# Performance work log

Measured on AMD Instinct MI355X. Metric: run time of the kernel, lower is better.

## Reference

```python
import jax, jax.numpy as jnp
import numpy as np

N_FFT = 1024
FREQ = N_FFT // 2 + 1          # 513
FRAMES = 256
WIN_MIN = 10.0                 # max(1, n_fft//100)
WIN_MAX = 1024.0               # n_fft
HOP_MIN = 1.0
HOP_MAX = 256.0
EPS = 1e-12
SIG_LEN = int(HOP_MAX) * FRAMES + N_FFT  # 66560


def setup_inputs() -> dict:
    key = jax.random.key(0)
    k1, k2, k3 = jax.random.split(key, 3)
    x = jax.random.normal(k1, (4, SIG_LEN), dtype=jnp.float32)
    raw_win_length = jax.random.normal(k2, (FREQ,), dtype=jnp.float32)
    raw_hop_length = jax.random.normal(k3, (1,), dtype=jnp.float32)
    return {"x": x, "raw_win_length": raw_win_length, "raw_hop_length": raw_hop_length}


def reference(x, raw_win_length, raw_hop_length):
    B, L = x.shape
    dt = x.dtype
    # sigmoid reparameterization (matches logit init in __init__)
    hop = HOP_MIN + jax.nn.sigmoid(raw_hop_length[0]) * (HOP_MAX - HOP_MIN)      # scalar
    theta = WIN_MIN + jax.nn.sigmoid(raw_win_length) * (WIN_MAX - WIN_MIN)

    # fractional frame positions: integer floor for gather, differentiable frac
    t = jnp.arange(FRAMES, dtype=dt)
    pos = jnp.clip(t * hop, 0.0, float(L - N_FFT))                               # [T]
    idx_floor = jnp.floor(pos).astype(jnp.int32)                                 # [T] (non-diff)
    idx_frac = pos - idx_floor.astype(dt)                                        # [T] (diff: d/dhop = t)

    # unfold: frames[b,t,n] = x[b, idx_floor[t] + n]
    n = jnp.arange(N_FFT)
    frames = x[:, idx_floor[:, None] + n[None, :]]                               # [B,T,N]

    # fractionally-shifted, per-frequency-length hann window: [F,T,N]
    nf = n.astype(dt)
    d = nf[None, :] - (N_FFT - 1) / 2.0 - idx_frac[:, None]                      # [T,N] offset from true center
    th = theta[:, None, None]                                                    # [F,1,1]
    w = jnp.where(jnp.abs(d)[None] <= th / 2.0,
                  0.5 + 0.5 * jnp.cos(2.0 * jnp.pi * d[None] / th),
                  0.0)                                                           # [F,T,N]

    # direct DFT (window varies per freq bin -> no FFT possible)
    k = jnp.arange(FREQ, dtype=dt)
    ang = 2.0 * jnp.pi * k[:, None] * nf[None, :] / N_FFT                        # [F,N]
    re = jnp.einsum('btn,ftn,fn->bft', frames, w, jnp.cos(ang))
    im = -jnp.einsum('btn,ftn,fn->bft', frames, w, jnp.sin(ang))
    stft = jax.lax.complex(re, im)                                               # [B,F,T]
    spec = jnp.abs(stft) + EPS                                                   # magnitude_power = 1
    return spec, stft
```

## Files before the change

### kernel.cpp

```cpp
#include <hip/hip_runtime.h>
#include <math.h>

#define NFFT   1024
#define FREQ   513
#define FRAMES 256
#define SIGLEN 66560
#define NB     4
#define BFT    (NB * FREQ * FRAMES)
#define NWAVE  4
#define NTHR   (64 * NWAVE)
#define NCHUNK 9
#define UNITS  (NCHUNK * FRAMES)

typedef float f32x2 __attribute__((ext_vector_type(2)));

__device__ __forceinline__ float sigmoid_f32(float v)
{
    if (v >= 0.0f) {
        return 1.0f / (1.0f + expf(-v));
    } else {
        const float e = expf(v);
        return e / (1.0f + e);
    }
}

__device__ __forceinline__ float rfl_f32(float v)
{
    return __int_as_float(__builtin_amdgcn_readfirstlane(__float_as_int(v)));
}

__global__ __launch_bounds__(1024)
void dstft_setup(const float* __restrict__ raw_win,
                 const float* __restrict__ raw_hop,
                 unsigned short* __restrict__ sf,
                 float* __restrict__ ctmax,
                 int* __restrict__ tbase,
                 float* __restrict__ tc)
{
    __shared__ float th[FREQ];
    const int tid = threadIdx.x;
    if (tid < FREQ)
        th[tid] = 10.0f + sigmoid_f32(raw_win[tid]) * 1014.0f;
    __syncthreads();
    if (tid < FREQ) {
        const float ti = th[tid];
        int r = 0;
        for (int j = 0; j < FREQ; ++j) {
            const float tj = th[j];
            r += (tj > ti) || (tj == ti && j < tid);
        }
        sf[r] = (unsigned short)tid;
        if ((r & 63) == 0) ctmax[r >> 6] = ti;
    }
    if (tid < FRAMES) {
        const float hop = 1.0f + sigmoid_f32(raw_hop[0]) * 255.0f;
        float pos = (float)tid * hop;
        pos = fminf(fmaxf(pos, 0.0f), 65536.0f);
        const float fl = floorf(pos);
        tbase[tid] = (int)fl;
        tc[tid]    = 511.5f + (pos - fl);
    }
}

__global__ __launch_bounds__(NTHR, 8)
void dstft_main(const float* __restrict__ x,
                const float* __restrict__ raw_win,
                const float* __restrict__ raw_hop,
                const unsigned short* __restrict__ sf,
                const float* __restrict__ ctmax,
                const int* __restrict__ tbase,
                const float* __restrict__ tc,
                float* __restrict__ out, int out_size, int stft_mode)
{
    const int tid  = threadIdx.x;
    const int lane = tid & 63;
    const int q    = tid >> 6;

    __shared__ __align__(16) unsigned char smem[NFFT * sizeof(float4)];
    float4* xlds = reinterpret_cast<float4*>(smem);
    float (*part)[64][9] = reinterpret_cast<float (*)[64][9]>(smem);

    const int u     = (int)blockIdx.x;
    const int chunk = u >> 8;
    const int t     = u & 255;
    const int spos  = chunk * 64 + lane;
    const bool active = (spos < FREQ);

    int   f = 0;
    float theta, tmax, c;
    int   base;

    if (sf) {
        if (active) {
            f = (int)sf[spos];
            f = (f < 0) ? 0 : ((f > FREQ - 1) ? (FREQ - 1) : f);
        }
        theta = active ? (10.0f + sigmoid_f32(raw_win[f]) * 1014.0f) : 10.0f;
        tmax  = rfl_f32(ctmax[chunk]);
        base  = __builtin_amdgcn_readfirstlane(tbase[t]);
        c     = rfl_f32(tc[t]);
    } else {
        if (active) f = spos;
        theta = active ? (10.0f + sigmoid_f32(raw_win[f]) * 1014.0f) : 10.0f;
        float tmaxv = theta;
#pragma unroll
        for (int s = 32; s; s >>= 1)
            tmaxv = fmaxf(tmaxv, __shfl_xor(tmaxv, s, 64));
        tmax = rfl_f32(tmaxv);
        const float hop = 1.0f + sigmoid_f32(raw_hop[0]) * 255.0f;
        float pos = (float)t * hop;
        pos = fminf(fmaxf(pos, 0.0f), 65536.0f);
        const float fl = floorf(pos);
        base = __builtin_amdgcn_readfirstlane((int)fl);
        c    = rfl_f32(511.5f + (pos - fl));
    }

    int lo = (int)floorf(c - 0.5f * tmax);
    int hi = (int)ceilf (c + 0.5f * tmax);
    lo = lo > 0 ? lo : 0;
    hi = hi < (NFFT - 1) ? hi : (NFFT - 1);
    int cnt = hi - lo + 1;
    cnt = cnt < 0 ? 0 : (cnt > NFFT ? NFFT : cnt);
    lo  = __builtin_amdgcn_readfirstlane(lo);
    cnt = __builtin_amdgcn_readfirstlane(cnt);

    for (int n = lo + tid; n < lo + cnt; n += NTHR) {
        float4 v;
        v.x = x[base + n];
        v.y = x[base + n + SIGLEN];
        v.z = x[base + n + 2 * SIGLEN];
        v.w = x[base + n + 3 * SIGLEN];
        xlds[n - lo] = v;
    }
    __syncthreads();

    const int s0     = lo + (cnt * q) / NWAVE;
    const int s1     = lo + (cnt * (q + 1)) / NWAVE;
    const int segcnt = s1 - s0;

    const float invth = 1.0f / theta;
    float r = ((float)s0 - c) * invth;

    const float sdr = (float)f * (1.0f / 1024.0f);
    const float cd  = __builtin_amdgcn_cosf(sdr);
    const float sd  = __builtin_amdgcn_sinf(sdr);
    int m0 = (f * s0) & (NFFT - 1);
    m0 = (m0 >= 512) ? (m0 - 1024) : m0;
    const float p0 = (float)m0 * (1.0f / 1024.0f);

    f32x2 p;
    p.x = __builtin_amdgcn_cosf(p0);
    p.y = __builtin_amdgcn_sinf(p0);
    const f32x2 cdv = { cd,  cd };
    const f32x2 sdv = { -sd, sd };

    f32x2 are01 = {0.f, 0.f}, are23 = {0.f, 0.f};
    f32x2 aim01 = {0.f, 0.f}, aim23 = {0.f, 0.f};

    const float4* __restrict__ xp = &xlds[s0 - lo];
#pragma unroll 4
    for (int i = 0; i < segcnt; ++i) {
        const float rc = __builtin_amdgcn_fmed3f(r, -0.5f, 0.5f);
        const float w  = fmaf(0.5f, __builtin_amdgcn_cosf(rc), 0.5f);
        const float wc  = w * p.x;
        const float wsn = w * p.y;
        const f32x2 wcv = { wc,  wc  };
        const f32x2 wsv = { wsn, wsn };
        const float4 v = xp[i];
        const f32x2 v01 = { v.x, v.y };
        const f32x2 v23 = { v.z, v.w };
        are01 = __builtin_elementwise_fma(v01, wcv, are01);
        are23 = __builtin_elementwise_fma(v23, wcv, are23);
        aim01 = __builtin_elementwise_fma(v01, wsv, aim01);
        aim23 = __builtin_elementwise_fma(v23, wsv, aim23);
        const f32x2 ps = p.yx;
        p = __builtin_elementwise_fma(p, cdv, ps * sdv);
        r += invth;
    }

    __syncthreads();
    part[q][lane][0] = are01.x;  part[q][lane][1] = are01.y;
    part[q][lane][2] = are23.x;  part[q][lane][3] = are23.y;
    part[q][lane][4] = aim01.x;  part[q][lane][5] = aim01.y;
    part[q][lane][6] = aim23.x;  part[q][lane][7] = aim23.y;
    __syncthreads();

    if (active) {
        float res = 0.f, sms = 0.f;
#pragma unroll
        for (int pw = 0; pw < NWAVE; ++pw) {
            res += part[pw][lane][q];
            sms += part[pw][lane][4 + q];
        }
        const float re = res;
        const float im = -sms;
        const int idx = q * (FREQ * FRAMES) + f * FRAMES + t;
        if (idx < out_size)
            out[idx] = sqrtf(fmaf(re, re, im * im)) + 1e-12f;
        if (stft_mode == 2) {
            if (BFT + 2 * idx + 1 < out_size) {
                out[BFT + 2 * idx]     = re;
                out[BFT + 2 * idx + 1] = im;
            }
        } else {
            if (BFT + idx < out_size)
                out[BFT + idx] = re;
        }
    }
}

extern "C" void kernel_launch(void* const* d_in, const int* in_sizes, int n_in,
                              void* d_out, int out_size, void* d_ws, size_t ws_size,
                              hipStream_t stream)
{
    const float* x       = (const float*)d_in[0];
    const float* raw_win = (const float*)d_in[1];
    const float* raw_hop = (const float*)d_in[2];
    float* out = (float*)d_out;

    unsigned short* sf    = nullptr;
    float*          ctmax = nullptr;
    int*            tbase = nullptr;
    float*          tc    = nullptr;
    if (d_ws != nullptr && ws_size >= 3200) {
        sf    = (unsigned short*)d_ws;
        ctmax = (float*)((char*)d_ws + 1028);
        tbase = (int*)  ((char*)d_ws + 1064);
        tc    = (float*)((char*)d_ws + 2088);
        dstft_setup<<<1, 1024, 0, stream>>>(raw_win, raw_hop,
                                            sf, ctmax, tbase, tc);
    }
    const int stft_mode = (out_size >= 3 * BFT) ? 2 : 1;
    dstft_main<<<UNITS, NTHR, 0, stream>>>(
        x, raw_win, raw_hop, sf, ctmax, tbase, tc, out, out_size, stft_mode);
}
```

Baseline: 56.83 us.

## Process two adjacent frames per block over a shared union span

Each block now computes two consecutive frames. It loads the union of both frames' sample ranges into LDS once, and a single twiddle recurrence indexed by absolute sample position is shared by both frames. Each frame's phase is then corrected by a per-frame rotation in the epilogue. This halves the grid and reuses the LDS loads and twiddle work across frames. In exchange, both frames iterate over the whole union span, which includes samples that fall outside one frame's window, so per-element cosine work doubles. The span is also clamped to 1280 entries, which could truncate data if the hop is near its maximum.

```diff
diff --git a/kernel.cpp b/kernel.cpp
--- a/kernel.cpp
+++ b/kernel.cpp
@@ -10,7 +10,9 @@
 #define NWAVE  4
 #define NTHR   (64 * NWAVE)
 #define NCHUNK 9
-#define UNITS  (NCHUNK * FRAMES)
+#define NPAIR  (FRAMES / 2)
+#define GRIDP  (NCHUNK * NPAIR)
+#define MAXU   1280
 
 typedef float f32x2 __attribute__((ext_vector_type(2)));
 
@@ -76,19 +78,20 @@
     const int lane = tid & 63;
     const int q    = tid >> 6;
 
-    __shared__ __align__(16) unsigned char smem[NFFT * sizeof(float4)];
+    __shared__ __align__(16) unsigned char smem[MAXU * sizeof(float4)];
     float4* xlds = reinterpret_cast<float4*>(smem);
-    float (*part)[64][9] = reinterpret_cast<float (*)[64][9]>(smem);
+    float (*part)[64][17] = reinterpret_cast<float (*)[64][17]>(smem);
 
     const int u     = (int)blockIdx.x;
-    const int chunk = u >> 8;
-    const int t     = u & 255;
+    const int chunk = u >> 7;
+    const int tp    = u & (NPAIR - 1);
+    const int t0    = 2 * tp, t1 = t0 + 1;
     const int spos  = chunk * 64 + lane;
     const bool active = (spos < FREQ);
 
     int   f = 0;
-    float theta, tmax, c;
-    int   base;
+    float theta, tmax, c0, c1;
+    int   base0, base1;
 
     if (sf) {
         if (active) {
@@ -97,8 +100,10 @@
         }
         theta = active ? (10.0f + sigmoid_f32(raw_win[f]) * 1014.0f) : 10.0f;
         tmax  = rfl_f32(ctmax[chunk]);
-        base  = __builtin_amdgcn_readfirstlane(tbase[t]);
-        c     = rfl_f32(tc[t]);
+        base0 = __builtin_amdgcn_readfirstlane(tbase[t0]);
+        base1 = __builtin_amdgcn_readfirstlane(tbase[t1]);
+        c0    = rfl_f32(tc[t0]);
+        c1    = rfl_f32(tc[t1]);
     } else {
         if (active) f = spos;
         theta = active ? (10.0f + sigmoid_f32(raw_win[f]) * 1014.0f) : 10.0f;
@@ -108,43 +113,49 @@
             tmaxv = fmaxf(tmaxv, __shfl_xor(tmaxv, s, 64));
         tmax = rfl_f32(tmaxv);
         const float hop = 1.0f + sigmoid_f32(raw_hop[0]) * 255.0f;
-        float pos = (float)t * hop;
-        pos = fminf(fmaxf(pos, 0.0f), 65536.0f);
-        const float fl = floorf(pos);
-        base = __builtin_amdgcn_readfirstlane((int)fl);
-        c    = rfl_f32(511.5f + (pos - fl));
-    }
-
-    int lo = (int)floorf(c - 0.5f * tmax);
-    int hi = (int)ceilf (c + 0.5f * tmax);
-    lo = lo > 0 ? lo : 0;
-    hi = hi < (NFFT - 1) ? hi : (NFFT - 1);
-    int cnt = hi - lo + 1;
-    cnt = cnt < 0 ? 0 : (cnt > NFFT ? NFFT : cnt);
-    lo  = __builtin_amdgcn_readfirstlane(lo);
-    cnt = __builtin_amdgcn_readfirstlane(cnt);
-
-    for (int n = lo + tid; n < lo + cnt; n += NTHR) {
+        float pos0 = fminf(fmaxf((float)t0 * hop, 0.0f), 65536.0f);
+        float pos1 = fminf(fmaxf((float)t1 * hop, 0.0f), 65536.0f);
+        const float fl0 = floorf(pos0), fl1 = floorf(pos1);
+        base0 = __builtin_amdgcn_readfirstlane((int)fl0);
+        base1 = __builtin_amdgcn_readfirstlane((int)fl1);
+        c0    = rfl_f32(511.5f + (pos0 - fl0));
+        c1    = rfl_f32(511.5f + (pos1 - fl1));
+    }
+
+    int lo0 = (int)floorf(c0 - 0.5f * tmax);
+    int hi1 = (int)ceilf (c1 + 0.5f * tmax);
+    lo0 = lo0 > 0 ? lo0 : 0;
+    hi1 = hi1 < (NFFT - 1) ? hi1 : (NFFT - 1);
+    int gmin = base0 + lo0;
+    int gmax = base1 + hi1;
+    int cntU = gmax - gmin + 1;
+    cntU = cntU < 1 ? 1 : (cntU > MAXU ? MAXU : cntU);
+    gmin = __builtin_amdgcn_readfirstlane(gmin);
+    cntU = __builtin_amdgcn_readfirstlane(cntU);
+
+    for (int n = tid; n < cntU; n += NTHR) {
         float4 v;
-        v.x = x[base + n];
-        v.y = x[base + n + SIGLEN];
-        v.z = x[base + n + 2 * SIGLEN];
-        v.w = x[base + n + 3 * SIGLEN];
-        xlds[n - lo] = v;
-    }
-    __syncthreads();
-
-    const int s0     = lo + (cnt * q) / NWAVE;
-    const int s1     = lo + (cnt * (q + 1)) / NWAVE;
-    const int segcnt = s1 - s0;
+        v.x = x[gmin + n];
+        v.y = x[gmin + n + SIGLEN];
+        v.z = x[gmin + n + 2 * SIGLEN];
+        v.w = x[gmin + n + 3 * SIGLEN];
+        xlds[n] = v;
+    }
+    __syncthreads();
+
+    const int si     = (cntU * q) / NWAVE;
+    const int si1    = (cntU * (q + 1)) / NWAVE;
+    const int segcnt = si1 - si;
+    const int sg     = gmin + si;
 
     const float invth = 1.0f / theta;
-    float r = ((float)s0 - c) * invth;
+    float r0 = ((float)(sg - base0) - c0) * invth;
+    float r1 = ((float)(sg - base1) - c1) * invth;
 
     const float sdr = (float)f * (1.0f / 1024.0f);
     const float cd  = __builtin_amdgcn_cosf(sdr);
     const float sd  = __builtin_amdgcn_sinf(sdr);
-    int m0 = (f * s0) & (NFFT - 1);
+    int m0 = (f * sg) & (NFFT - 1);
     m0 = (m0 >= 512) ? (m0 - 1024) : m0;
     const float p0 = (float)m0 * (1.0f / 1024.0f);
 
@@ -154,57 +165,78 @@
     const f32x2 cdv = { cd,  cd };
     const f32x2 sdv = { -sd, sd };
 
-    f32x2 are01 = {0.f, 0.f}, are23 = {0.f, 0.f};
-    f32x2 aim01 = {0.f, 0.f}, aim23 = {0.f, 0.f};
-
-    const float4* __restrict__ xp = &xlds[s0 - lo];
-#pragma unroll 4
+    f32x2 cr0a = {0,0}, cr0b = {0,0}, sr0a = {0,0}, sr0b = {0,0};
+    f32x2 cr1a = {0,0}, cr1b = {0,0}, sr1a = {0,0}, sr1b = {0,0};
+
+    const float4* __restrict__ xp = &xlds[si];
+#pragma unroll 2
     for (int i = 0; i < segcnt; ++i) {
-        const float rc = __builtin_amdgcn_fmed3f(r, -0.5f, 0.5f);
-        const float w  = fmaf(0.5f, __builtin_amdgcn_cosf(rc), 0.5f);
-        const float wc  = w * p.x;
-        const float wsn = w * p.y;
-        const f32x2 wcv = { wc,  wc  };
-        const f32x2 wsv = { wsn, wsn };
+        const float rc0 = __builtin_amdgcn_fmed3f(r0, -0.5f, 0.5f);
+        const float w0  = fmaf(0.5f, __builtin_amdgcn_cosf(rc0), 0.5f);
+        const float rc1 = __builtin_amdgcn_fmed3f(r1, -0.5f, 0.5f);
+        const float w1  = fmaf(0.5f, __builtin_amdgcn_cosf(rc1), 0.5f);
         const float4 v = xp[i];
-        const f32x2 v01 = { v.x, v.y };
-        const f32x2 v23 = { v.z, v.w };
-        are01 = __builtin_elementwise_fma(v01, wcv, are01);
-        are23 = __builtin_elementwise_fma(v23, wcv, are23);
-        aim01 = __builtin_elementwise_fma(v01, wsv, aim01);
-        aim23 = __builtin_elementwise_fma(v23, wsv, aim23);
+        const f32x2 va = { v.x, v.y };
+        const f32x2 vb = { v.z, v.w };
+        const float wc0 = w0 * p.x, ws0 = w0 * p.y;
+        const float wc1 = w1 * p.x, ws1 = w1 * p.y;
+        const f32x2 wc0v = { wc0, wc0 }, ws0v = { ws0, ws0 };
+        const f32x2 wc1v = { wc1, wc1 }, ws1v = { ws1, ws1 };
+        cr0a = __builtin_elementwise_fma(va, wc0v, cr0a);
+        cr0b = __builtin_elementwise_fma(vb, wc0v, cr0b);
+        sr0a = __builtin_elementwise_fma(va, ws0v, sr0a);
+        sr0b = __builtin_elementwise_fma(vb, ws0v, sr0b);
+        cr1a = __builtin_elementwise_fma(va, wc1v, cr1a);
+        cr1b = __builtin_elementwise_fma(vb, wc1v, cr1b);
+        sr1a = __builtin_elementwise_fma(va, ws1v, sr1a);
+        sr1b = __builtin_elementwise_fma(vb, ws1v, sr1b);
         const f32x2 ps = p.yx;
         p = __builtin_elementwise_fma(p, cdv, ps * sdv);
-        r += invth;
-    }
-
-    __syncthreads();
-    part[q][lane][0] = are01.x;  part[q][lane][1] = are01.y;
-    part[q][lane][2] = are23.x;  part[q][lane][3] = are23.y;
-    part[q][lane][4] = aim01.x;  part[q][lane][5] = aim01.y;
-    part[q][lane][6] = aim23.x;  part[q][lane][7] = aim23.y;
+        r0 += invth;
+        r1 += invth;
+    }
+
+    __syncthreads();
+    part[q][lane][0]  = cr0a.x;  part[q][lane][1]  = cr0a.y;
+    part[q][lane][2]  = cr0b.x;  part[q][lane][3]  = cr0b.y;
+    part[q][lane][4]  = sr0a.x;  part[q][lane][5]  = sr0a.y;
+    part[q][lane][6]  = sr0b.x;  part[q][lane][7]  = sr0b.y;
+    part[q][lane][8]  = cr1a.x;  part[q][lane][9]  = cr1a.y;
+    part[q][lane][10] = cr1b.x;  part[q][lane][11] = cr1b.y;
+    part[q][lane][12] = sr1a.x;  part[q][lane][13] = sr1a.y;
+    part[q][lane][14] = sr1b.x;  part[q][lane][15] = sr1b.y;
     __syncthreads();
 
     if (active) {
-        float res = 0.f, sms = 0.f;
 #pragma unroll
-        for (int pw = 0; pw < NWAVE; ++pw) {
-            res += part[pw][lane][q];
-            sms += part[pw][lane][4 + q];
-        }
-        const float re = res;
-        const float im = -sms;
-        const int idx = q * (FREQ * FRAMES) + f * FRAMES + t;
-        if (idx < out_size)
-            out[idx] = sqrtf(fmaf(re, re, im * im)) + 1e-12f;
-        if (stft_mode == 2) {
-            if (BFT + 2 * idx + 1 < out_size) {
-                out[BFT + 2 * idx]     = re;
-                out[BFT + 2 * idx + 1] = im;
+        for (int k = 0; k < 2; ++k) {
+            float cr = 0.f, sr = 0.f;
+#pragma unroll
+            for (int pw = 0; pw < NWAVE; ++pw) {
+                cr += part[pw][lane][8 * k + q];
+                sr += part[pw][lane][8 * k + 4 + q];
             }
-        } else {
-            if (BFT + idx < out_size)
-                out[BFT + idx] = re;
+            const int bk = k ? base1 : base0;
+            int mk = (f * bk) & (NFFT - 1);
+            mk = (mk >= 512) ? (mk - 1024) : mk;
+            const float ph = (float)mk * (1.0f / 1024.0f);
+            const float cph = __builtin_amdgcn_cosf(ph);
+            const float sph = __builtin_amdgcn_sinf(ph);
+            const float re = cr * cph + sr * sph;
+            const float im = cr * sph - sr * cph;
+            const int tk  = k ? t1 : t0;
+            const int idx = q * (FREQ * FRAMES) + f * FRAMES + tk;
+            if (idx < out_size)
+                out[idx] = sqrtf(fmaf(re, re, im * im)) + 1e-12f;
+            if (stft_mode == 2) {
+                if (BFT + 2 * idx + 1 < out_size) {
+                    out[BFT + 2 * idx]     = re;
+                    out[BFT + 2 * idx + 1] = im;
+                }
+            } else {
+                if (BFT + idx < out_size)
+                    out[BFT + idx] = re;
+            }
         }
     }
 }
@@ -231,6 +263,6 @@
                                             sf, ctmax, tbase, tc);
     }
     const int stft_mode = (out_size >= 3 * BFT) ? 2 : 1;
-    dstft_main<<<UNITS, NTHR, 0, stream>>>(
+    dstft_main<<<GRIDP, NTHR, 0, stream>>>(
         x, raw_win, raw_hop, sf, ctmax, tbase, tc, out, out_size, stft_mode);
 }
```

New measurement: 67.71 us. 19.2% more time.

## Replace LDS staging of signal with per-wave global loads and readlane broadcast

Applied to the files above, without the earlier changes.

Removes the LDS staging buffer and the block barrier that followed the cooperative load. Each wave now loads 64 consecutive samples for all four batches into registers and broadcasts them to every lane with readlane inside a fully unrolled 64-step loop. Groups of 64 samples are interleaved across waves, and the twiddle phase is re-seeded with cos/sin at the start of each group. In exchange it adds four readlane ops per sample, drops the packed 2-wide FMAs, and the last partial group runs full 64-step iterations on clamped duplicate samples.

```diff
diff --git a/kernel.cpp b/kernel.cpp
--- a/kernel.cpp
+++ b/kernel.cpp
@@ -12,8 +12,6 @@
 #define NCHUNK 9
 #define UNITS  (NCHUNK * FRAMES)
 
-typedef float f32x2 __attribute__((ext_vector_type(2)));
-
 __device__ __forceinline__ float sigmoid_f32(float v)
 {
     if (v >= 0.0f) {
@@ -27,6 +25,11 @@
 __device__ __forceinline__ float rfl_f32(float v)
 {
     return __int_as_float(__builtin_amdgcn_readfirstlane(__float_as_int(v)));
+}
+
+__device__ __forceinline__ float rdlane_f32(float v, int k)
+{
+    return __uint_as_float(__builtin_amdgcn_readlane(__float_as_uint(v), k));
 }
 
 __global__ __launch_bounds__(1024)
@@ -76,9 +79,7 @@
     const int lane = tid & 63;
     const int q    = tid >> 6;
 
-    __shared__ __align__(16) unsigned char smem[NFFT * sizeof(float4)];
-    float4* xlds = reinterpret_cast<float4*>(smem);
-    float (*part)[64][9] = reinterpret_cast<float (*)[64][9]>(smem);
+    __shared__ float part[NWAVE][64][9];
 
     const int u     = (int)blockIdx.x;
     const int chunk = u >> 8;
@@ -123,66 +124,60 @@
     cnt = cnt < 0 ? 0 : (cnt > NFFT ? NFFT : cnt);
     lo  = __builtin_amdgcn_readfirstlane(lo);
     cnt = __builtin_amdgcn_readfirstlane(cnt);
-
-    for (int n = lo + tid; n < lo + cnt; n += NTHR) {
-        float4 v;
-        v.x = x[base + n];
-        v.y = x[base + n + SIGLEN];
-        v.z = x[base + n + 2 * SIGLEN];
-        v.w = x[base + n + 3 * SIGLEN];
-        xlds[n - lo] = v;
-    }
-    __syncthreads();
-
-    const int s0     = lo + (cnt * q) / NWAVE;
-    const int s1     = lo + (cnt * (q + 1)) / NWAVE;
-    const int segcnt = s1 - s0;
+    const int his = lo + cnt - 1;
+    const int G   = (cnt + 63) >> 6;
 
     const float invth = 1.0f / theta;
-    float r = ((float)s0 - c) * invth;
-
     const float sdr = (float)f * (1.0f / 1024.0f);
     const float cd  = __builtin_amdgcn_cosf(sdr);
     const float sd  = __builtin_amdgcn_sinf(sdr);
-    int m0 = (f * s0) & (NFFT - 1);
-    m0 = (m0 >= 512) ? (m0 - 1024) : m0;
-    const float p0 = (float)m0 * (1.0f / 1024.0f);
-
-    f32x2 p;
-    p.x = __builtin_amdgcn_cosf(p0);
-    p.y = __builtin_amdgcn_sinf(p0);
-    const f32x2 cdv = { cd,  cd };
-    const f32x2 sdv = { -sd, sd };
-
-    f32x2 are01 = {0.f, 0.f}, are23 = {0.f, 0.f};
-    f32x2 aim01 = {0.f, 0.f}, aim23 = {0.f, 0.f};
-
-    const float4* __restrict__ xp = &xlds[s0 - lo];
-#pragma unroll 4
-    for (int i = 0; i < segcnt; ++i) {
-        const float rc = __builtin_amdgcn_fmed3f(r, -0.5f, 0.5f);
-        const float w  = fmaf(0.5f, __builtin_amdgcn_cosf(rc), 0.5f);
-        const float wc  = w * p.x;
-        const float wsn = w * p.y;
-        const f32x2 wcv = { wc,  wc  };
-        const f32x2 wsv = { wsn, wsn };
-        const float4 v = xp[i];
-        const f32x2 v01 = { v.x, v.y };
-        const f32x2 v23 = { v.z, v.w };
-        are01 = __builtin_elementwise_fma(v01, wcv, are01);
-        are23 = __builtin_elementwise_fma(v23, wcv, are23);
-        aim01 = __builtin_elementwise_fma(v01, wsv, aim01);
-        aim23 = __builtin_elementwise_fma(v23, wsv, aim23);
-        const f32x2 ps = p.yx;
-        p = __builtin_elementwise_fma(p, cdv, ps * sdv);
-        r += invth;
-    }
-
-    __syncthreads();
-    part[q][lane][0] = are01.x;  part[q][lane][1] = are01.y;
-    part[q][lane][2] = are23.x;  part[q][lane][3] = are23.y;
-    part[q][lane][4] = aim01.x;  part[q][lane][5] = aim01.y;
-    part[q][lane][6] = aim23.x;  part[q][lane][7] = aim23.y;
+
+    float re0 = 0.f, re1 = 0.f, re2 = 0.f, re3 = 0.f;
+    float im0 = 0.f, im1 = 0.f, im2 = 0.f, im3 = 0.f;
+
+#pragma unroll 1
+    for (int g = q; g < G; g += NWAVE) {
+        const int sg = lo + (g << 6);
+        int sidx = sg + lane;
+        sidx = sidx < his ? sidx : his;
+        const float* __restrict__ xa = x + base + sidx;
+        const float xb0 = xa[0];
+        const float xb1 = xa[SIGLEN];
+        const float xb2 = xa[2 * SIGLEN];
+        const float xb3 = xa[3 * SIGLEN];
+
+        const float rg = ((float)sg - c) * invth;
+        int m0 = (f * sg) & (NFFT - 1);
+        m0 = (m0 >= 512) ? (m0 - 1024) : m0;
+        const float p0 = (float)m0 * (1.0f / 1024.0f);
+        float pc = __builtin_amdgcn_cosf(p0);
+        float ps = __builtin_amdgcn_sinf(p0);
+
+#pragma unroll
+        for (int k = 0; k < 64; ++k) {
+            const float x0 = rdlane_f32(xb0, k);
+            const float x1 = rdlane_f32(xb1, k);
+            const float x2 = rdlane_f32(xb2, k);
+            const float x3 = rdlane_f32(xb3, k);
+            const float rk = fmaf((float)k, invth, rg);
+            const float rc = __builtin_amdgcn_fmed3f(rk, -0.5f, 0.5f);
+            const float w  = fmaf(0.5f, __builtin_amdgcn_cosf(rc), 0.5f);
+            const float wc = w * pc;
+            const float ws = w * ps;
+            re0 = fmaf(x0, wc, re0);  im0 = fmaf(x0, ws, im0);
+            re1 = fmaf(x1, wc, re1);  im1 = fmaf(x1, ws, im1);
+            re2 = fmaf(x2, wc, re2);  im2 = fmaf(x2, ws, im2);
+            re3 = fmaf(x3, wc, re3);  im3 = fmaf(x3, ws, im3);
+            const float npc = fmaf(pc, cd, -(ps * sd));
+            const float nps = fmaf(ps, cd,   pc * sd);
+            pc = npc; ps = nps;
+        }
+    }
+
+    part[q][lane][0] = re0;  part[q][lane][1] = re1;
+    part[q][lane][2] = re2;  part[q][lane][3] = re3;
+    part[q][lane][4] = im0;  part[q][lane][5] = im1;
+    part[q][lane][6] = im2;  part[q][lane][7] = im3;
     __syncthreads();
 
     if (active) {
```

Result: slower. 71.73 us (+26.2%).

## Use persistent blocks with an atomic work counter for dynamic load balancing

Applied to the files above, without the earlier changes.

Launches a fixed grid of 2048 persistent blocks that pull (chunk, frame) work units from a global atomic counter, which the setup kernel initialises. Units with wide windows cost far more than narrow ones, so dynamic scheduling is meant to even out the tail and cut block launch overhead. It adds an atomic per unit and an extra barrier per iteration, and relies on the workspace being present.

```diff
diff --git a/kernel.cpp b/kernel.cpp
--- a/kernel.cpp
+++ b/kernel.cpp
@@ -11,6 +11,7 @@
 #define NTHR   (64 * NWAVE)
 #define NCHUNK 9
 #define UNITS  (NCHUNK * FRAMES)
+#define GRIDD  2048
 
 typedef float f32x2 __attribute__((ext_vector_type(2)));
 
@@ -35,10 +36,12 @@
                  unsigned short* __restrict__ sf,
                  float* __restrict__ ctmax,
                  int* __restrict__ tbase,
-                 float* __restrict__ tc)
+                 float* __restrict__ tc,
+                 int* __restrict__ counter)
 {
     __shared__ float th[FREQ];
     const int tid = threadIdx.x;
+    if (tid == 0) *counter = GRIDD;
     if (tid < FREQ)
         th[tid] = 10.0f + sigmoid_f32(raw_win[tid]) * 1014.0f;
     __syncthreads();
@@ -70,6 +73,7 @@
                 const float* __restrict__ ctmax,
                 const int* __restrict__ tbase,
                 const float* __restrict__ tc,
+                int* __restrict__ counter,
                 float* __restrict__ out, int out_size, int stft_mode)
 {
     const int tid  = threadIdx.x;
@@ -79,133 +83,149 @@
     __shared__ __align__(16) unsigned char smem[NFFT * sizeof(float4)];
     float4* xlds = reinterpret_cast<float4*>(smem);
     float (*part)[64][9] = reinterpret_cast<float (*)[64][9]>(smem);
-
-    const int u     = (int)blockIdx.x;
-    const int chunk = u >> 8;
-    const int t     = u & 255;
-    const int spos  = chunk * 64 + lane;
-    const bool active = (spos < FREQ);
-
-    int   f = 0;
-    float theta, tmax, c;
-    int   base;
-
-    if (sf) {
+    __shared__ int u_next[2];
+
+    const bool dyn = (counter != nullptr);
+    int u   = (int)blockIdx.x;
+    int tog = 0;
+
+    while (u < UNITS) {
+        if (dyn && tid == 0) u_next[tog] = atomicAdd(counter, 1);
+
+        const int chunk = u >> 8;
+        const int t     = u & 255;
+        const int spos  = chunk * 64 + lane;
+        const bool active = (spos < FREQ);
+
+        int   f = 0;
+        float theta, tmax, c;
+        int   base;
+
+        if (sf) {
+            if (active) {
+                f = (int)sf[spos];
+                f = (f < 0) ? 0 : ((f > FREQ - 1) ? (FREQ - 1) : f);
+            }
+            theta = active ? (10.0f + sigmoid_f32(raw_win[f]) * 1014.0f)
+                           : 10.0f;
+            tmax  = rfl_f32(ctmax[chunk]);
+            base  = __builtin_amdgcn_readfirstlane(tbase[t]);
+            c     = rfl_f32(tc[t]);
+        } else {
+            if (active) f = spos;
+            theta = active ? (10.0f + sigmoid_f32(raw_win[f]) * 1014.0f)
+                           : 10.0f;
+            float tmaxv = theta;
+#pragma unroll
+            for (int s = 32; s; s >>= 1)
+                tmaxv = fmaxf(tmaxv, __shfl_xor(tmaxv, s, 64));
+            tmax = rfl_f32(tmaxv);
+            const float hop = 1.0f + sigmoid_f32(raw_hop[0]) * 255.0f;
+            float pos = (float)t * hop;
+            pos = fminf(fmaxf(pos, 0.0f), 65536.0f);
+            const float fl = floorf(pos);
+            base = __builtin_amdgcn_readfirstlane((int)fl);
+            c    = rfl_f32(511.5f + (pos - fl));
+        }
+
+        int lo = (int)floorf(c - 0.5f * tmax);
+        int hi = (int)ceilf (c + 0.5f * tmax);
+        lo = lo > 0 ? lo : 0;
+        hi = hi < (NFFT - 1) ? hi : (NFFT - 1);
+        int cnt = hi - lo + 1;
+        cnt = cnt < 0 ? 0 : (cnt > NFFT ? NFFT : cnt);
+        lo  = __builtin_amdgcn_readfirstlane(lo);
+        cnt = __builtin_amdgcn_readfirstlane(cnt);
+
+        __syncthreads();
+
+        for (int n = lo + tid; n < lo + cnt; n += NTHR) {
+            float4 v;
+            v.x = x[base + n];
+            v.y = x[base + n + SIGLEN];
+            v.z = x[base + n + 2 * SIGLEN];
+            v.w = x[base + n + 3 * SIGLEN];
+            xlds[n - lo] = v;
+        }
+        __syncthreads();
+
+        const int s0     = lo + (cnt * q) / NWAVE;
+        const int s1     = lo + (cnt * (q + 1)) / NWAVE;
+        const int segcnt = s1 - s0;
+
+        const float invth = 1.0f / theta;
+        float r = ((float)s0 - c) * invth;
+
+        const float sdr = (float)f * (1.0f / 1024.0f);
+        const float cd  = __builtin_amdgcn_cosf(sdr);
+        const float sd  = __builtin_amdgcn_sinf(sdr);
+        int m0 = (f * s0) & (NFFT - 1);
+        m0 = (m0 >= 512) ? (m0 - 1024) : m0;
+        const float p0 = (float)m0 * (1.0f / 1024.0f);
+
+        f32x2 p;
+        p.x = __builtin_amdgcn_cosf(p0);
+        p.y = __builtin_amdgcn_sinf(p0);
+        const f32x2 cdv = { cd,  cd };
+        const f32x2 sdv = { -sd, sd };
+
+        f32x2 are01 = {0.f, 0.f}, are23 = {0.f, 0.f};
+        f32x2 aim01 = {0.f, 0.f}, aim23 = {0.f, 0.f};
+
+        const float4* __restrict__ xp = &xlds[s0 - lo];
+#pragma unroll 4
+        for (int i = 0; i < segcnt; ++i) {
+            const float rc = __builtin_amdgcn_fmed3f(r, -0.5f, 0.5f);
+            const float w  = fmaf(0.5f, __builtin_amdgcn_cosf(rc), 0.5f);
+            const float wc  = w * p.x;
+            const float wsn = w * p.y;
+            const f32x2 wcv = { wc,  wc  };
+            const f32x2 wsv = { wsn, wsn };
+            const float4 v = xp[i];
+            const f32x2 v01 = { v.x, v.y };
+            const f32x2 v23 = { v.z, v.w };
+            are01 = __builtin_elementwise_fma(v01, wcv, are01);
+            are23 = __builtin_elementwise_fma(v23, wcv, are23);
+            aim01 = __builtin_elementwise_fma(v01, wsv, aim01);
+            aim23 = __builtin_elementwise_fma(v23, wsv, aim23);
+            const f32x2 ps = p.yx;
+            p = __builtin_elementwise_fma(p, cdv, ps * sdv);
+            r += invth;
+        }
+
+        __syncthreads();
+        part[q][lane][0] = are01.x;  part[q][lane][1] = are01.y;
+        part[q][lane][2] = are23.x;  part[q][lane][3] = are23.y;
+        part[q][lane][4] = aim01.x;  part[q][lane][5] = aim01.y;
+        part[q][lane][6] = aim23.x;  part[q][lane][7] = aim23.y;
+        __syncthreads();
+
         if (active) {
-            f = (int)sf[spos];
-            f = (f < 0) ? 0 : ((f > FREQ - 1) ? (FREQ - 1) : f);
-        }
-        theta = active ? (10.0f + sigmoid_f32(raw_win[f]) * 1014.0f) : 10.0f;
-        tmax  = rfl_f32(ctmax[chunk]);
-        base  = __builtin_amdgcn_readfirstlane(tbase[t]);
-        c     = rfl_f32(tc[t]);
-    } else {
-        if (active) f = spos;
-        theta = active ? (10.0f + sigmoid_f32(raw_win[f]) * 1014.0f) : 10.0f;
-        float tmaxv = theta;
+            float res = 0.f, sms = 0.f;
 #pragma unroll
-        for (int s = 32; s; s >>= 1)
-            tmaxv = fmaxf(tmaxv, __shfl_xor(tmaxv, s, 64));
-        tmax = rfl_f32(tmaxv);
-        const float hop = 1.0f + sigmoid_f32(raw_hop[0]) * 255.0f;
-        float pos = (float)t * hop;
-        pos = fminf(fmaxf(pos, 0.0f), 65536.0f);
-        const float fl = floorf(pos);
-        base = __builtin_amdgcn_readfirstlane((int)fl);
-        c    = rfl_f32(511.5f + (pos - fl));
-    }
-
-    int lo = (int)floorf(c - 0.5f * tmax);
-    int hi = (int)ceilf (c + 0.5f * tmax);
-    lo = lo > 0 ? lo : 0;
-    hi = hi < (NFFT - 1) ? hi : (NFFT - 1);
-    int cnt = hi - lo + 1;
-    cnt = cnt < 0 ? 0 : (cnt > NFFT ? NFFT : cnt);
-    lo  = __builtin_amdgcn_readfirstlane(lo);
-    cnt = __builtin_amdgcn_readfirstlane(cnt);
-
-    for (int n = lo + tid; n < lo + cnt; n += NTHR) {
-        float4 v;
-        v.x = x[base + n];
-        v.y = x[base + n + SIGLEN];
-        v.z = x[base + n + 2 * SIGLEN];
-        v.w = x[base + n + 3 * SIGLEN];
-        xlds[n - lo] = v;
-    }
-    __syncthreads();
-
-    const int s0     = lo + (cnt * q) / NWAVE;
-    const int s1     = lo + (cnt * (q + 1)) / NWAVE;
-    const int segcnt = s1 - s0;
-
-    const float invth = 1.0f / theta;
-    float r = ((float)s0 - c) * invth;
-
-    const float sdr = (float)f * (1.0f / 1024.0f);
-    const float cd  = __builtin_amdgcn_cosf(sdr);
-    const float sd  = __builtin_amdgcn_sinf(sdr);
-    int m0 = (f * s0) & (NFFT - 1);
-    m0 = (m0 >= 512) ? (m0 - 1024) : m0;
-    const float p0 = (float)m0 * (1.0f / 1024.0f);
-
-    f32x2 p;
-    p.x = __builtin_amdgcn_cosf(p0);
-    p.y = __builtin_amdgcn_sinf(p0);
-    const f32x2 cdv = { cd,  cd };
-    const f32x2 sdv = { -sd, sd };
-
-    f32x2 are01 = {0.f, 0.f}, are23 = {0.f, 0.f};
-    f32x2 aim01 = {0.f, 0.f}, aim23 = {0.f, 0.f};
-
-    const float4* __restrict__ xp = &xlds[s0 - lo];
-#pragma unroll 4
-    for (int i = 0; i < segcnt; ++i) {
-        const float rc = __builtin_amdgcn_fmed3f(r, -0.5f, 0.5f);
-        const float w  = fmaf(0.5f, __builtin_amdgcn_cosf(rc), 0.5f);
-        const float wc  = w * p.x;
-        const float wsn = w * p.y;
-        const f32x2 wcv = { wc,  wc  };
-        const f32x2 wsv = { wsn, wsn };
-        const float4 v = xp[i];
-        const f32x2 v01 = { v.x, v.y };
-        const f32x2 v23 = { v.z, v.w };
-        are01 = __builtin_elementwise_fma(v01, wcv, are01);
-        are23 = __builtin_elementwise_fma(v23, wcv, are23);
-        aim01 = __builtin_elementwise_fma(v01, wsv, aim01);
-        aim23 = __builtin_elementwise_fma(v23, wsv, aim23);
-        const f32x2 ps = p.yx;
-        p = __builtin_elementwise_fma(p, cdv, ps * sdv);
-        r += invth;
-    }
-
-    __syncthreads();
-    part[q][lane][0] = are01.x;  part[q][lane][1] = are01.y;
-    part[q][lane][2] = are23.x;  part[q][lane][3] = are23.y;
-    part[q][lane][4] = aim01.x;  part[q][lane][5] = aim01.y;
-    part[q][lane][6] = aim23.x;  part[q][lane][7] = aim23.y;
-    __syncthreads();
-
-    if (active) {
-        float res = 0.f, sms = 0.f;
-#pragma unroll
-        for (int pw = 0; pw < NWAVE; ++pw) {
-            res += part[pw][lane][q];
-            sms += part[pw][lane][4 + q];
-        }
-        const float re = res;
-        const float im = -sms;
-        const int idx = q * (FREQ * FRAMES) + f * FRAMES + t;
-        if (idx < out_size)
-            out[idx] = sqrtf(fmaf(re, re, im * im)) + 1e-12f;
-        if (stft_mode == 2) {
-            if (BFT + 2 * idx + 1 < out_size) {
-                out[BFT + 2 * idx]     = re;
-                out[BFT + 2 * idx + 1] = im;
+            for (int pw = 0; pw < NWAVE; ++pw) {
+                res += part[pw][lane][q];
+                sms += part[pw][lane][4 + q];
             }
-        } else {
-            if (BFT + idx < out_size)
-                out[BFT + idx] = re;
-        }
+            const float re = res;
+            const float im = -sms;
+            const int idx = q * (FREQ * FRAMES) + f * FRAMES + t;
+            if (idx < out_size)
+                out[idx] = sqrtf(fmaf(re, re, im * im)) + 1e-12f;
+            if (stft_mode == 2) {
+                if (BFT + 2 * idx + 1 < out_size) {
+                    out[BFT + 2 * idx]     = re;
+                    out[BFT + 2 * idx + 1] = im;
+                }
+            } else {
+                if (BFT + idx < out_size)
+                    out[BFT + idx] = re;
+            }
+        }
+
+        if (!dyn) break;
+        u = u_next[tog];
+        tog ^= 1;
     }
 }
 
@@ -222,15 +242,19 @@
     float*          ctmax = nullptr;
     int*            tbase = nullptr;
     float*          tc    = nullptr;
+    int*            cnt   = nullptr;
     if (d_ws != nullptr && ws_size >= 3200) {
         sf    = (unsigned short*)d_ws;
         ctmax = (float*)((char*)d_ws + 1028);
         tbase = (int*)  ((char*)d_ws + 1064);
         tc    = (float*)((char*)d_ws + 2088);
+        cnt   = (int*)  ((char*)d_ws + 3136);
         dstft_setup<<<1, 1024, 0, stream>>>(raw_win, raw_hop,
-                                            sf, ctmax, tbase, tc);
+                                            sf, ctmax, tbase, tc, cnt);
     }
     const int stft_mode = (out_size >= 3 * BFT) ? 2 : 1;
-    dstft_main<<<UNITS, NTHR, 0, stream>>>(
-        x, raw_win, raw_hop, sf, ctmax, tbase, tc, out, out_size, stft_mode);
-}
+    const int grid = cnt ? GRIDD : UNITS;
+    dstft_main<<<grid, NTHR, 0, stream>>>(
+        x, raw_win, raw_hop, sf, ctmax, tbase, tc, cnt,
+        out, out_size, stft_mode);
+}
```

Measured after the change: 80.17 us. 1.41x slower.
